# Performance work log

Measured on AMD Instinct MI355X. Metric: run time of the kernel, lower is better.

Reference implementation:

```python
import jax, jax.numpy as jnp
import numpy as np

SMOOTH = 1e-3
EPS = 1e-12


def setup_inputs() -> dict:
    key = jax.random.key(0)
    k1, k2, k3 = jax.random.split(key, 3)
    pred = jax.random.normal(k1, (1, 16, 384, 384), dtype=jnp.float32)
    labels = jax.random.randint(k2, (1, 16, 384, 384), 0, 2, dtype=jnp.int32)
    # stand-in for create_table_neighbour_code_to_surface_area((1,1,1)): 256-entry LUT
    area = jax.random.uniform(k3, (256,), dtype=jnp.float32) * 2.0
    return {"pred": pred, "labels": labels, "area": area}


def _corners(x2):
    # x2: (B, 2, Y+2, X+2) zero-padded slice pair -> (B, 8, (Y+1)*(X+1))
    # corner index k = dz*4 + dy*2 + dx, matching torch unfold(kernel=(2,2), padding=1)
    B, _, Yp, Xp = x2.shape
    Y, X = Yp - 1, Xp - 1
    cs = [x2[:, dz, dy:dy + Y, dx:dx + X]
          for dz in (0, 1) for dy in (0, 1) for dx in (0, 1)]
    return jnp.stack(cs, axis=1).reshape(B, 8, Y * X)


def _surface_dice(pred_sig, labels, area, smooth):
    B, Z, Y, X = pred_sig.shape
    # bases[i, k] = bit k of code i  (== [c=='1' for c in f'{i:08b}'[::-1]])
    bits = jnp.arange(8, dtype=jnp.int32)
    bases = ((jnp.arange(256, dtype=jnp.int32)[:, None] >> bits[None, :]) & 1).astype(jnp.float32)  # (256,8)
    n_bits = bases.sum(1)  # (256,) popcount

    # blank zero slices on both z ends + the unfold's zero padding in y/x
    Pp = jnp.pad(pred_sig, ((0, 0), (1, 1), (1, 1), (1, 1)))
    Lp = jnp.pad(labels.astype(jnp.int32), ((0, 0), (1, 1), (1, 1), (1, 1)))

    def pair(carry, i):
        num, den, vol = carry
        pz = jax.lax.dynamic_slice(Pp, (0, i, 0, 0), (B, 2, Y + 2, X + 2))
        lz = jax.lax.dynamic_slice(Lp, (0, i, 0, 0), (B, 2, Y + 2, X + 2))
        pc = _corners(pz)                      # (B, 8, Np) float
        lc = _corners(lz)                      # (B, 8, Np) int32
        byte = jnp.left_shift(lc, bits[None, :, None]).sum(axis=1)  # (B, Np) label corner code

        # basis_weights = 1 - mean_k (pc_k - bases_ik)^2, expanded so the
        # (B,256,8,Np) broadcast is never materialized
        sp2 = jnp.sum(pc * pc, axis=1)                       # (B, Np)
        cross = jnp.einsum('bkn,ik->bin', pc, bases)         # (B, 256, Np)
        bw = 1.0 - (sp2[:, None, :] + n_bits[None, :, None] - 2.0 * cross) / 8.0

        pred_byte = jnp.argmax(bw, axis=1)                   # (B, Np)
        pred_area = area[pred_byte]                          # (B, Np)
        label_area = area[byte]                              # (B, Np)
        pw = jnp.take_along_axis(bw, byte[:, None, :], axis=1)[:, 0]  # (B, Np)

        # binary_cross_entropy(unfolded_pred, unfolded_labels) per element
        lf = lc.astype(jnp.float32)
        logp = jnp.log(jnp.maximum(pc, EPS))
        log1mp = jnp.log(jnp.maximum(1.0 - pc, EPS))
        bce = -(lf * logp + (1.0 - lf) * log1mp)             # (B, 8, Np)
        interior = (byte == 0) | (byte == 255)               # (B, Np)
        v = jnp.where(interior[:, None, :], bce, 0.0).mean((1, 2))

        inter = jnp.sum(pw * label_area, axis=1)
        return (num + 2.0 * inter,
                den + label_area.sum(1) + pred_area.sum(1),
                vol + v), None

    init = (jnp.zeros((B,), jnp.float32), jnp.zeros((B,), jnp.float32), jnp.zeros((B,), jnp.float32))
    (num, den, vol), _ = jax.lax.scan(pair, init, jnp.arange(Z + 1))
    dice = 1.0 - (num + smooth) / (den + smooth)
    return dice.mean() + vol.mean()


def reference(pred, labels, area):
    return _surface_dice(jax.nn.sigmoid(pred), labels, area, SMOOTH)
```

## Files before the change

### kernel.cpp

```cpp
#include <hip/hip_runtime.h>
#include <math.h>

constexpr int ZN = 16, YN = 384, XN = 384;
constexpr int NZ = 17, NY = 385, NX = 385;
constexpr int NP = NY * NX;
constexpr int NROWS = NZ * NY;
constexpr int BLOCKS = (NROWS + 3) / 4;

__device__ __forceinline__ float sigm(float p) {
    return __fdividef(1.f, 1.f + __expf(-p));
}

__global__ __launch_bounds__(256) void sd_main(
        const float* __restrict__ pred,
        const int*   __restrict__ labels,
        const float* __restrict__ area,
        float*       __restrict__ partial)
{
    __shared__ float s_area[256];
    {
        const int t = threadIdx.x;
        const int own = t >> 4, prv = t & 15;
        int code = 0;
#pragma unroll
        for (int r = 0; r < 4; ++r)
            code |= (((prv >> r) & 1) << (2 * r)) | (((own >> r) & 1) << (2 * r + 1));
        s_area[t] = area[code];
    }
    __syncthreads();

    const int lane = threadIdx.x & 63;
    const int wid = __builtin_amdgcn_readfirstlane(blockIdx.x * 4 + (threadIdx.x >> 6));

    float num = 0.f, den = 0.f, vol = 0.f;

    if (wid < NROWS) {
        const int z = wid / NY;
        const int y = wid - z * NY;

        bool rv[4]; int cbase[4];
#pragma unroll
        for (int r = 0; r < 4; ++r) {
            const int zz = z - 1 + (r >> 1);
            const int yy = y - 1 + (r & 1);
            rv[r] = ((unsigned)zz < (unsigned)ZN) & ((unsigned)yy < (unsigned)YN);
            const int zc = min(max(zz, 0), ZN - 1);
            const int yc = min(max(yy, 0), YN - 1);
            cbase[r] = (zc * YN + yc) * XN;
        }

        float p[6][4]; int li[6][4];
#pragma unroll
        for (int j = 0; j < 6; ++j) {
            const int xo = j * 64 + lane;
#pragma unroll
            for (int r = 0; r < 4; ++r) {
                p[j][r]  = pred[cbase[r] + xo];
                li[j][r] = labels[cbase[r] + xo];
            }
        }

        float S[6][4]; float Q[6]; int B[6];
#pragma unroll
        for (int j = 0; j < 6; ++j) {
            Q[j] = 0.f; B[j] = 0;
#pragma unroll
            for (int r = 0; r < 4; ++r) {
                float sv = sigm(p[j][r]);
                sv = rv[r] ? sv : 0.f;
                const int lm = rv[r] ? li[j][r] : 0;
                S[j][r] = sv;
                const float d = sv - (float)lm;
                Q[j] = fmaf(d, d, Q[j]);
                B[j] |= (lm << r) | ((int)(sv > 0.5f) << (r + 4));
            }
        }

        auto node = [&](const float* sp, float qp, int bp,
                        const float* so, float qo, int bo) {
            const int idxL = ((bo & 15) << 4) | (bp & 15);
            const int idxP = (bo & 0xF0) | (bp >> 4);
            const float la = s_area[idxL];
            const float pa = s_area[idxP];
            num = fmaf(2.f * la, 1.f - (qp + qo) * 0.125f, num);
            den += la + pa;
            if (idxL == 0 || idxL == 255) {
                const bool one = (idxL == 255);
                float b = 0.f;
#pragma unroll
                for (int r = 0; r < 4; ++r) {
                    b += __logf(fmaxf(one ? sp[r] : 1.f - sp[r], 1e-12f))
                       + __logf(fmaxf(one ? so[r] : 1.f - so[r], 1e-12f));
                }
                vol -= b;
            }
        };

        const int src = (lane + 63) & 63;
        const bool l0 = (lane == 0);
        float rp_s[4] = {0.f, 0.f, 0.f, 0.f};
        float rp_q = 0.f; int rp_b = 0;
#pragma unroll
        for (int j = 0; j < 6; ++j) {
            float ps[4], pq; int pb;
#pragma unroll
            for (int r = 0; r < 4; ++r) {
                const float ro = __shfl(S[j][r], src);
                ps[r] = l0 ? rp_s[r] : ro;
                rp_s[r] = ro;
            }
            {
                const float ro = __shfl(Q[j], src);
                pq = l0 ? rp_q : ro;
                rp_q = ro;
            }
            {
                const int ro = __shfl(B[j], src);
                pb = l0 ? rp_b : ro;
                rp_b = ro;
            }
            node(ps, pq, pb, S[j], Q[j], B[j]);
        }
        if (lane == 63) {
            const float zs[4] = {0.f, 0.f, 0.f, 0.f};
            node(S[5], Q[5], B[5], zs, 0.f, 0);
        }
    }

#pragma unroll
    for (int off = 32; off > 0; off >>= 1) {
        num += __shfl_down(num, off);
        den += __shfl_down(den, off);
        vol += __shfl_down(vol, off);
    }
    __shared__ float rn[4], rd[4], rvv[4];
    const int w = threadIdx.x >> 6;
    if (lane == 0) { rn[w] = num; rd[w] = den; rvv[w] = vol; }
    __syncthreads();
    if (threadIdx.x == 0) {
        partial[blockIdx.x]              = rn[0] + rn[1] + rn[2] + rn[3];
        partial[BLOCKS + blockIdx.x]     = rd[0] + rd[1] + rd[2] + rd[3];
        partial[2 * BLOCKS + blockIdx.x] = rvv[0] + rvv[1] + rvv[2] + rvv[3];
    }
}

__global__ __launch_bounds__(256) void sd_final(
        const float* __restrict__ partial, float* __restrict__ out)
{
    double n = 0.0, d = 0.0, v = 0.0;
    for (int b = threadIdx.x; b < BLOCKS; b += 256) {
        n += (double)partial[b];
        d += (double)partial[BLOCKS + b];
        v += (double)partial[2 * BLOCKS + b];
    }
#pragma unroll
    for (int off = 32; off > 0; off >>= 1) {
        n += __shfl_down(n, off);
        d += __shfl_down(d, off);
        v += __shfl_down(v, off);
    }
    __shared__ double sn[4], sd_[4], sv[4];
    const int lane = threadIdx.x & 63, w = threadIdx.x >> 6;
    if (lane == 0) { sn[w] = n; sd_[w] = d; sv[w] = v; }
    __syncthreads();
    if (threadIdx.x == 0) {
        const double num = sn[0] + sn[1] + sn[2] + sn[3];
        const double den = sd_[0] + sd_[1] + sd_[2] + sd_[3];
        const double vol = (sv[0] + sv[1] + sv[2] + sv[3]) / (8.0 * (double)NP);
        const double dice = 1.0 - (num + 1e-3) / (den + 1e-3);
        out[0] = (float)(dice + vol);
    }
}

extern "C" void kernel_launch(void* const* d_in, const int* in_sizes, int n_in,
                              void* d_out, int out_size, void* d_ws, size_t ws_size,
                              hipStream_t stream)
{
    const float* pred   = (const float*)d_in[0];
    const int*   labels = (const int*)d_in[1];
    const float* area   = (const float*)d_in[2];
    float* out     = (float*)d_out;
    float* partial = (float*)d_ws;

    sd_main<<<BLOCKS, 256, 0, stream>>>(pred, labels, area, partial);
    sd_final<<<1, 256, 0, stream>>>(partial, out);
}
```

Measured before the change: 86.22 us.

## Process two output rows per wave and vectorize loads to float2

Each wave now handles a pair of y-rows, loading 3 input rows per z-slice (6 total) instead of 4 rows per single output row, so the shared middle row is reused. Each lane also processes two adjacent x positions with 8-byte vector loads, which halves the cross-lane shuffles per output node. The intent is to cut redundant global loads and sigmoid evaluations. In exchange, per-thread register pressure is higher and there are fewer waves overall, which may lower occupancy and latency hiding.

```diff
diff --git a/kernel.cpp b/kernel.cpp
--- a/kernel.cpp
+++ b/kernel.cpp
@@ -4,8 +4,12 @@
 constexpr int ZN = 16, YN = 384, XN = 384;
 constexpr int NZ = 17, NY = 385, NX = 385;
 constexpr int NP = NY * NX;
-constexpr int NROWS = NZ * NY;
-constexpr int BLOCKS = (NROWS + 3) / 4;
+constexpr int NPAIRS = 193;
+constexpr int NWAVES = NZ * NPAIRS;
+constexpr int BLOCKS = (NWAVES + 3) / 4;
+
+typedef float F2 __attribute__((ext_vector_type(2)));
+typedef int   I2 __attribute__((ext_vector_type(2)));
 
 __device__ __forceinline__ float sigm(float p) {
     return __fdividef(1.f, 1.f + __expf(-p));
@@ -34,52 +38,31 @@
 
     float num = 0.f, den = 0.f, vol = 0.f;
 
-    if (wid < NROWS) {
-        const int z = wid / NY;
-        const int y = wid - z * NY;
-
-        bool rv[4]; int cbase[4];
-#pragma unroll
-        for (int r = 0; r < 4; ++r) {
-            const int zz = z - 1 + (r >> 1);
-            const int yy = y - 1 + (r & 1);
-            rv[r] = ((unsigned)zz < (unsigned)ZN) & ((unsigned)yy < (unsigned)YN);
-            const int zc = min(max(zz, 0), ZN - 1);
-            const int yc = min(max(yy, 0), YN - 1);
-            cbase[r] = (zc * YN + yc) * XN;
-        }
-
-        float p[6][4]; int li[6][4];
-#pragma unroll
-        for (int j = 0; j < 6; ++j) {
-            const int xo = j * 64 + lane;
-#pragma unroll
-            for (int r = 0; r < 4; ++r) {
-                p[j][r]  = pred[cbase[r] + xo];
-                li[j][r] = labels[cbase[r] + xo];
-            }
-        }
-
-        float S[6][4]; float Q[6]; int B[6];
-#pragma unroll
-        for (int j = 0; j < 6; ++j) {
-            Q[j] = 0.f; B[j] = 0;
-#pragma unroll
-            for (int r = 0; r < 4; ++r) {
-                float sv = sigm(p[j][r]);
-                sv = rv[r] ? sv : 0.f;
-                const int lm = rv[r] ? li[j][r] : 0;
-                S[j][r] = sv;
-                const float d = sv - (float)lm;
-                Q[j] = fmaf(d, d, Q[j]);
-                B[j] |= (lm << r) | ((int)(sv > 0.5f) << (r + 4));
-            }
-        }
-
-        auto node = [&](const float* sp, float qp, int bp,
-                        const float* so, float qo, int bo) {
-            const int idxL = ((bo & 15) << 4) | (bp & 15);
-            const int idxP = (bo & 0xF0) | (bp >> 4);
+    if (wid < NWAVES) {
+        const int z = wid / NPAIRS;
+        const int u = wid - z * NPAIRS;
+        const bool hasB = (u < 192);
+
+        bool rv[6]; int cbase[6];
+#pragma unroll
+        for (int zi = 0; zi < 2; ++zi)
+#pragma unroll
+            for (int gi = 0; gi < 3; ++gi) {
+                const int r = zi * 3 + gi;
+                const int zz = z - 1 + zi, yy = 2 * u - 1 + gi;
+                rv[r] = ((unsigned)zz < (unsigned)ZN) & ((unsigned)yy < (unsigned)YN);
+                const int zc = min(max(zz, 0), ZN - 1);
+                const int yc = min(max(yy, 0), YN - 1);
+                cbase[r] = (zc * YN + yc) * XN;
+            }
+
+        auto nibA = [](int b) { return (b & 3) | ((b >> 1) & 12); };
+        auto nibB = [](int b) { return ((b >> 1) & 3) | ((b >> 2) & 12); };
+
+        auto node = [&](const float* sp, float qp, int lp, int pp,
+                        const float* so, float qo, int lo, int po) {
+            const int idxL = (lo << 4) | lp;
+            const int idxP = (po << 4) | pp;
             const float la = s_area[idxL];
             const float pa = s_area[idxP];
             num = fmaf(2.f * la, 1.f - (qp + qo) * 0.125f, num);
@@ -98,32 +81,64 @@
 
         const int src = (lane + 63) & 63;
         const bool l0 = (lane == 0);
-        float rp_s[4] = {0.f, 0.f, 0.f, 0.f};
-        float rp_q = 0.f; int rp_b = 0;
-#pragma unroll
-        for (int j = 0; j < 6; ++j) {
-            float ps[4], pq; int pb;
-#pragma unroll
-            for (int r = 0; r < 4; ++r) {
-                const float ro = __shfl(S[j][r], src);
-                ps[r] = l0 ? rp_s[r] : ro;
-                rp_s[r] = ro;
-            }
-            {
-                const float ro = __shfl(Q[j], src);
-                pq = l0 ? rp_q : ro;
-                rp_q = ro;
-            }
-            {
-                const int ro = __shfl(B[j], src);
-                pb = l0 ? rp_b : ro;
-                rp_b = ro;
-            }
-            node(ps, pq, pb, S[j], Q[j], B[j]);
-        }
-        if (lane == 63) {
-            const float zs[4] = {0.f, 0.f, 0.f, 0.f};
-            node(S[5], Q[5], B[5], zs, 0.f, 0);
+        float crs[6] = {0.f, 0.f, 0.f, 0.f, 0.f, 0.f};
+        float crqA = 0.f, crqB = 0.f; int crb = 0;
+
+#pragma unroll
+        for (int c = 0; c < 3; ++c) {
+            const int xo = c * 128 + 2 * lane;
+            float s0[6], s1[6], dq0[6], dq1[6];
+            int b0 = 0, b1 = 0;
+#pragma unroll
+            for (int r = 0; r < 6; ++r) {
+                const F2 p2 = *(const F2*)(pred + cbase[r] + xo);
+                const I2 l2 = *(const I2*)(labels + cbase[r] + xo);
+                float sv0 = sigm(p2.x), sv1 = sigm(p2.y);
+                sv0 = rv[r] ? sv0 : 0.f;
+                sv1 = rv[r] ? sv1 : 0.f;
+                const int lm0 = rv[r] ? l2.x : 0;
+                const int lm1 = rv[r] ? l2.y : 0;
+                s0[r] = sv0; s1[r] = sv1;
+                const float d0 = sv0 - (float)lm0, d1 = sv1 - (float)lm1;
+                dq0[r] = d0 * d0; dq1[r] = d1 * d1;
+                b0 |= (lm0 << r) | ((int)(sv0 > 0.5f) << (8 + r));
+                b1 |= (lm1 << r) | ((int)(sv1 > 0.5f) << (8 + r));
+            }
+            const float qA0 = dq0[0] + dq0[1] + dq0[3] + dq0[4];
+            const float qB0 = dq0[1] + dq0[2] + dq0[4] + dq0[5];
+            const float qA1 = dq1[0] + dq1[1] + dq1[3] + dq1[4];
+            const float qB1 = dq1[1] + dq1[2] + dq1[4] + dq1[5];
+
+            float rs[6]; float rqA, rqB; int rb;
+#pragma unroll
+            for (int r = 0; r < 6; ++r) {
+                const float ro = __shfl(s1[r], src);
+                rs[r] = l0 ? crs[r] : ro;
+                crs[r] = ro;
+            }
+            { const float ro = __shfl(qA1, src); rqA = l0 ? crqA : ro; crqA = ro; }
+            { const float ro = __shfl(qB1, src); rqB = l0 ? crqB : ro; crqB = ro; }
+            { const int   ro = __shfl(b1,  src); rb  = l0 ? crb  : ro; crb  = ro; }
+
+            const float rA[4] = { rs[0], rs[1], rs[3], rs[4] };
+            const float rB[4] = { rs[1], rs[2], rs[4], rs[5] };
+            const float A0[4] = { s0[0], s0[1], s0[3], s0[4] };
+            const float B0[4] = { s0[1], s0[2], s0[4], s0[5] };
+            const float A1[4] = { s1[0], s1[1], s1[3], s1[4] };
+            const float B1[4] = { s1[1], s1[2], s1[4], s1[5] };
+
+            node(rA, rqA, nibA(rb), nibA(rb >> 8), A0, qA0, nibA(b0), nibA(b0 >> 8));
+            node(A0, qA0, nibA(b0), nibA(b0 >> 8), A1, qA1, nibA(b1), nibA(b1 >> 8));
+            if (hasB) {
+                node(rB, rqB, nibB(rb), nibB(rb >> 8), B0, qB0, nibB(b0), nibB(b0 >> 8));
+                node(B0, qB0, nibB(b0), nibB(b0 >> 8), B1, qB1, nibB(b1), nibB(b1 >> 8));
+            }
+            if (c == 2 && lane == 63) {
+                const float zs[4] = {0.f, 0.f, 0.f, 0.f};
+                node(A1, qA1, nibA(b1), nibA(b1 >> 8), zs, 0.f, 0, 0);
+                if (hasB)
+                    node(B1, qB1, nibB(b1), nibB(b1 >> 8), zs, 0.f, 0, 0);
+            }
         }
     }
 
```

After: 88.03 us. 1.02x slower.
